# Kernel tuning notes

Hardware: AMD Instinct MI355X
Metric: run time of the kernel (lower is better)

The kernel has to match this reference:

```python
import jax, jax.numpy as jnp
import numpy as np

DIM = 256
HEADS = 4
HEAD_DIM = DIM // HEADS
SCALE = HEAD_DIM ** -0.5


def setup_inputs() -> dict:
    key = jax.random.key(0)
    k_x, k_wqkv, k_bqkv, k_wp, k_bp = jax.random.split(key, 5)
    B, N = 8, 2048
    x = jax.random.normal(k_x, (B, N, DIM), dtype=jnp.float32)
    # torch nn.Linear weights: [out_features, in_features]
    W_qkv = jax.random.normal(k_wqkv, (3 * DIM, DIM), dtype=jnp.float32) * (DIM ** -0.5)
    b_qkv = jax.random.normal(k_bqkv, (3 * DIM,), dtype=jnp.float32) * 0.02
    W_proj = jax.random.normal(k_wp, (DIM, DIM), dtype=jnp.float32) * (DIM ** -0.5)
    b_proj = jax.random.normal(k_bp, (DIM,), dtype=jnp.float32) * 0.02
    return {"x": x, "W_qkv": W_qkv, "b_qkv": b_qkv, "W_proj": W_proj, "b_proj": b_proj}


def reference(x, W_qkv, b_qkv, W_proj, b_proj):
    B, N, C = x.shape
    h, d = HEADS, HEAD_DIM
    # fused QKV projection: [B,N,3C] -> [3,B,h,N,d]
    qkv = (jnp.einsum('bnc,oc->bno', x, W_qkv) + b_qkv)
    qkv = qkv.reshape(B, N, 3, h, d).transpose(2, 0, 3, 1, 4)
    q, k, v = qkv[0], qkv[1], qkv[2]
    # full N x N score matrix, as in the original module
    attn = jnp.einsum('bhnd,bhmd->bhnm', q, k) * SCALE
    attn = jax.nn.softmax(attn, axis=-1)
    out = jnp.einsum('bhnm,bhmd->bhnd', attn, v)  # [B,h,N,d]
    out = out.transpose(0, 2, 1, 3).reshape(B, N, C)
    return jnp.einsum('bnc,oc->bno', out, W_proj) + b_proj
```

## Files before the change

kernel.cpp:

```cpp
#include <hip/hip_runtime.h>
#include <hip/hip_bf16.h>


typedef __bf16 bf16x8 __attribute__((ext_vector_type(8)));
typedef float f32x4 __attribute__((ext_vector_type(4)));
typedef float f32x16 __attribute__((ext_vector_type(16)));
typedef unsigned u32x2 __attribute__((ext_vector_type(2)));

#define MFMA16(a, b, c) __builtin_amdgcn_mfma_f32_16x16x32_bf16((a), (b), (c), 0, 0, 0)
#define MFMA32(a, b, c) __builtin_amdgcn_mfma_f32_32x32x16_bf16((a), (b), (c), 0, 0, 0)

#define C2 0.18033688011112042f

#if __has_builtin(__builtin_amdgcn_exp2f)
__device__ __forceinline__ float fexp2(float x) { return __builtin_amdgcn_exp2f(x); }
#else
__device__ __forceinline__ float fexp2(float x) {
    float r;
    asm("v_exp_f32 %0, %1" : "=v"(r) : "v"(x));
    return r;
}
#endif

__device__ __forceinline__ bf16x8 ldg8(const __bf16* p) {
    return *reinterpret_cast<const bf16x8*>(p);
}

__device__ __forceinline__ bf16x8 cvt8(const float* p) {
    const f32x4 a = *reinterpret_cast<const f32x4*>(p);
    const f32x4 b = *reinterpret_cast<const f32x4*>(p + 4);
    bf16x8 r;
    r[0] = (__bf16)a[0]; r[1] = (__bf16)a[1]; r[2] = (__bf16)a[2]; r[3] = (__bf16)a[3];
    r[4] = (__bf16)b[0]; r[5] = (__bf16)b[1]; r[6] = (__bf16)b[2]; r[7] = (__bf16)b[3];
    return r;
}

__device__ __forceinline__ unsigned pk2(float a, float b) {
    __bf16 x = (__bf16)a, y = (__bf16)b;
    unsigned short ux = __builtin_bit_cast(unsigned short, x);
    unsigned short uy = __builtin_bit_cast(unsigned short, y);
    return (unsigned)ux | ((unsigned)uy << 16);
}

__global__ __launch_bounds__(256) void cvt_all(
    const float* __restrict__ X, const float* __restrict__ Wq,
    const float* __restrict__ Wp, __bf16* __restrict__ Xb,
    __bf16* __restrict__ Wqb, __bf16* __restrict__ Wpb)
{
    const int g = blockIdx.x * 256 + threadIdx.x;
    const float* src;
    __bf16* dst;
    int off;
    if (g < 524288)      { src = X;  dst = Xb;  off = g; }
    else if (g < 548864) { src = Wq; dst = Wqb; off = g - 524288; }
    else                 { src = Wp; dst = Wpb; off = g - 548864; }
    *reinterpret_cast<bf16x8*>(dst + (size_t)off * 8) = cvt8(src + (size_t)off * 8);
}

__global__ __launch_bounds__(256) void qkv_gemm(
    const __bf16* __restrict__ X, const __bf16* __restrict__ Wq,
    const float* __restrict__ bq, __bf16* __restrict__ Qw,
    __bf16* __restrict__ Kw, __bf16* __restrict__ Vt)
{
    const int tid = threadIdx.x;
    const int w = tid >> 6, lane = tid & 63;
    const int lo = lane & 15, hi = lane >> 4;
    const int n0 = blockIdx.x * 128;
    const int m0 = blockIdx.y * 128 + w * 32;

    f32x4 acc[2][8] = {};
    const __bf16* xp = X + (m0 + lo) * 256 + hi * 8;
    const __bf16* wp = Wq + (n0 + lo) * 256 + hi * 8;
    #pragma unroll
    for (int k = 0; k < 256; k += 32) {
        bf16x8 a0 = ldg8(xp + k);
        bf16x8 a1 = ldg8(xp + 16 * 256 + k);
        #pragma unroll
        for (int f = 0; f < 8; ++f) {
            bf16x8 bf = ldg8(wp + f * 16 * 256 + k);
            acc[0][f] = MFMA16(a0, bf, acc[0][f]);
            acc[1][f] = MFMA16(a1, bf, acc[1][f]);
        }
    }

    #pragma unroll
    for (int ni = 0; ni < 8; ++ni) {
        const int col = n0 + ni * 16 + lo;
        const float bias = bq[col];
        const float scale = (col < 256) ? C2 : 1.0f;
        #pragma unroll
        for (int mi = 0; mi < 2; ++mi) {
            #pragma unroll
            for (int r = 0; r < 4; ++r) {
                const int row = m0 + mi * 16 + hi * 4 + r;
                const __bf16 hv = (__bf16)((acc[mi][ni][r] + bias) * scale);
                const int bb = row >> 11, n = row & 2047;
                const int d = col & 63;
                if (col < 256) {
                    const int h = col >> 6;
                    Qw[((bb * 4 + h) * 2048 + n) * 64 + d] = hv;
                } else if (col < 512) {
                    const int h = (col - 256) >> 6;
                    Kw[((bb * 4 + h) * 2048 + n) * 64 + d] = hv;
                } else {
                    const int h = (col - 512) >> 6;
                    Vt[((bb * 4 + h) * 64 + d) * 2048 + n] = hv;
                }
            }
        }
    }
}

__global__ __launch_bounds__(512, 4) void attn_kernel(
    const __bf16* __restrict__ Qw, const __bf16* __restrict__ Kw,
    const __bf16* __restrict__ Vt, __bf16* __restrict__ Opart,
    float* __restrict__ Lbuf)
{
    __shared__ __align__(16) char lds[33280];

    const int tid = threadIdx.x;
    const int w = tid >> 6, lane = tid & 63;
    const int l31 = lane & 31, hi5 = lane >> 5;
    const int sw = w & 3;
    const int g  = w >> 2;

    const int bid = blockIdx.x;
    const int work = (bid & 7) * 128 + (bid >> 3);
    const int bh = work >> 5;
    const int split = (work >> 4) & 1;
    const int qx = work & 15;

    const int q = qx * 128 + sw * 32 + l31;
    const int kvbase = split * 1024 + g * 512;
    const int gbase = g * 16384;

    const __bf16* Qp = Qw + (bh * 2048 + q) * 64 + hi5 * 8;
    bf16x8 Qf[4];
    #pragma unroll
    for (int db = 0; db < 4; ++db) Qf[db] = ldg8(Qp + db * 16);

    const __bf16* Kbase = Kw + (size_t)bh * 2048 * 64;
    const __bf16* Vbase = Vt + (size_t)bh * 64 * 2048;

    const int idx = tid & 255;
    const int krow = idx >> 3, kcol8 = (idx & 7) * 8;
    const int swz = ((idx >> 3) & 7) << 4;
    const int kb0 = gbase + ((idx * 16) ^ swz);
    const int kb1 = gbase + (((idx + 256) * 16) ^ swz);
    const int vb0 = gbase + 8192 + ((idx * 16) ^ swz);
    const int vb1 = gbase + 8192 + (((idx + 256) * 16) ^ swz);

    bf16x8 R0 = ldg8(Kbase + (kvbase + krow) * 64 + kcol8);
    bf16x8 R1 = ldg8(Kbase + (kvbase + krow + 32) * 64 + kcol8);
    bf16x8 R2 = ldg8(Vbase + krow * 2048 + kvbase + kcol8);
    bf16x8 R3 = ldg8(Vbase + (krow + 32) * 2048 + kvbase + kcol8);

    f32x16 oacc0 = (f32x16)0.0f, oacc1 = (f32x16)0.0f;
    float lr = 0.0f;

    for (int t = 0; t < 8; ++t) {
        *reinterpret_cast<bf16x8*>(lds + kb0) = R0;
        *reinterpret_cast<bf16x8*>(lds + kb1) = R1;
        *reinterpret_cast<bf16x8*>(lds + vb0) = R2;
        *reinterpret_cast<bf16x8*>(lds + vb1) = R3;
        __syncthreads();

        if (t < 7) {
            const int kv0n = kvbase + (t + 1) * 64;
            R0 = ldg8(Kbase + (kv0n + krow) * 64 + kcol8);
            R1 = ldg8(Kbase + (kv0n + krow + 32) * 64 + kcol8);
            R2 = ldg8(Vbase + krow * 2048 + kv0n + kcol8);
            R3 = ldg8(Vbase + (krow + 32) * 2048 + kv0n + kcol8);
        }

        f32x16 s0 = (f32x16)0.0f, s1 = (f32x16)0.0f;
        #pragma unroll
        for (int db = 0; db < 4; ++db) {
            const int colb = hi5 * 16 + db * 32;
            bf16x8 k0 = *reinterpret_cast<const bf16x8*>(
                lds + gbase + ((l31 * 128 + colb) ^ ((l31 & 7) << 4)));
            bf16x8 k1 = *reinterpret_cast<const bf16x8*>(
                lds + gbase + (((l31 + 32) * 128 + colb) ^ ((l31 & 7) << 4)));
            s0 = MFMA32(k0, Qf[db], s0);
            s1 = MFMA32(k1, Qf[db], s1);
        }

        float p0[16], p1[16];
        #pragma unroll
        for (int i = 0; i < 16; ++i) p0[i] = fexp2(s0[i]);
        #pragma unroll
        for (int i = 0; i < 16; ++i) p1[i] = fexp2(s1[i]);

        float r0 = 0.f, r1 = 0.f, r2 = 0.f, r3 = 0.f;
        #pragma unroll
        for (int i = 0; i < 4; ++i) {
            r0 += p0[i]; r1 += p0[4 + i]; r2 += p0[8 + i]; r3 += p0[12 + i];
            r0 += p1[i]; r1 += p1[4 + i]; r2 += p1[8 + i]; r3 += p1[12 + i];
        }
        lr += (r0 + r1) + (r2 + r3);

#define PVSTEP(PARR, KH)                                                      \
        {                                                                     \
            _Pragma("unroll")                                                 \
            for (int bb2 = 0; bb2 < 2; ++bb2) {                               \
                const int vcolb = KH * 64 + bb2 * 32 + hi5 * 16;              \
                bf16x8 v0 = *reinterpret_cast<const bf16x8*>(                 \
                    lds + gbase + 8192 + ((l31 * 128 + vcolb) ^ ((l31 & 7) << 4))); \
                bf16x8 v1 = *reinterpret_cast<const bf16x8*>(                 \
                    lds + gbase + 8192 + (((l31 + 32) * 128 + vcolb) ^ ((l31 & 7) << 4))); \
                unsigned w0 = pk2(PARR[8 * bb2 + 0], PARR[8 * bb2 + 1]);      \
                unsigned w1 = pk2(PARR[8 * bb2 + 2], PARR[8 * bb2 + 3]);      \
                unsigned w2 = pk2(PARR[8 * bb2 + 4], PARR[8 * bb2 + 5]);      \
                unsigned w3 = pk2(PARR[8 * bb2 + 6], PARR[8 * bb2 + 7]);      \
                asm volatile("v_permlane32_swap_b32 %0, %1" : "+v"(w0), "+v"(w2)); \
                asm volatile("v_permlane32_swap_b32 %0, %1" : "+v"(w1), "+v"(w3)); \
                union { unsigned u[4]; bf16x8 v; } pb;                        \
                pb.u[0] = w0; pb.u[1] = w1; pb.u[2] = w2; pb.u[3] = w3;       \
                oacc0 = MFMA32(v0, pb.v, oacc0);                              \
                oacc1 = MFMA32(v1, pb.v, oacc1);                              \
            }                                                                 \
        }
        PVSTEP(p0, 0)
        PVSTEP(p1, 1)
#undef PVSTEP
        __syncthreads();
    }

    lr += __shfl_xor(lr, 32);

    float* mb = reinterpret_cast<float*>(lds);
    float* lb = reinterpret_cast<float*>(lds + 32768);
    if (g == 1) {
        #pragma unroll
        for (int i = 0; i < 16; ++i) {
            const int r = (i & 3) + 8 * (i >> 2) + 4 * hi5;
            mb[(sw * 64 + r) * 32 + l31] = oacc0[i];
            mb[(sw * 64 + 32 + r) * 32 + l31] = oacc1[i];
        }
        if (hi5 == 0) lb[sw * 32 + l31] = lr;
    }
    __syncthreads();
    if (g == 0) {
        #pragma unroll
        for (int i = 0; i < 16; ++i) {
            const int r = (i & 3) + 8 * (i >> 2) + 4 * hi5;
            oacc0[i] += mb[(sw * 64 + r) * 32 + l31];
            oacc1[i] += mb[(sw * 64 + 32 + r) * 32 + l31];
        }
        lr += lb[sw * 32 + l31];

        __bf16* Od = Opart + ((size_t)(split * 32 + bh) * 2048 + q) * 64 + hi5 * 4;
#define EPI(OACC, DBLK)                                                       \
        {                                                                     \
            _Pragma("unroll")                                                 \
            for (int rq = 0; rq < 4; ++rq) {                                  \
                u32x2 st;                                                     \
                st.x = pk2(OACC[rq * 4 + 0], OACC[rq * 4 + 1]);               \
                st.y = pk2(OACC[rq * 4 + 2], OACC[rq * 4 + 3]);               \
                *reinterpret_cast<u32x2*>(Od + DBLK * 32 + rq * 8) = st;      \
            }                                                                 \
        }
        EPI(oacc0, 0)
        EPI(oacc1, 1)
#undef EPI
        if (hi5 == 0) Lbuf[(size_t)(split * 32 + bh) * 2048 + q] = lr;
    }
}

__global__ __launch_bounds__(256) void merge_kernel(
    const __bf16* __restrict__ Opart, const float* __restrict__ Lbuf,
    __bf16* __restrict__ Ow)
{
    const int g = blockIdx.x * 256 + threadIdx.x;
    const int dg = g & 7;
    const int q = (g >> 3) & 2047;
    const int bh = g >> 14;
    const float l1 = Lbuf[(size_t)bh * 2048 + q];
    const float l2 = Lbuf[(size_t)(32 + bh) * 2048 + q];
    const float inv = 1.0f / (l1 + l2);
    const __bf16* O1 = Opart + ((size_t)bh * 2048 + q) * 64 + dg * 8;
    const __bf16* O2 = O1 + (size_t)32 * 2048 * 64;
    const bf16x8 a = ldg8(O1);
    const bf16x8 b = ldg8(O2);
    bf16x8 r;
    #pragma unroll
    for (int i = 0; i < 8; ++i)
        r[i] = (__bf16)(((float)a[i] + (float)b[i]) * inv);
    const int bb = bh >> 2, h = bh & 3;
    *reinterpret_cast<bf16x8*>(Ow + ((size_t)(bb * 2048 + q)) * 256 + h * 64 + dg * 8) = r;
}

__global__ __launch_bounds__(256) void proj_gemm(
    const __bf16* __restrict__ A, const __bf16* __restrict__ Wp,
    const float* __restrict__ bp, float* __restrict__ out)
{
    const int tid = threadIdx.x;
    const int w = tid >> 6, lane = tid & 63;
    const int lo = lane & 15, hi = lane >> 4;
    const int n0 = blockIdx.x * 128;
    const int m0 = blockIdx.y * 128 + w * 32;

    f32x4 acc[2][8] = {};
    const __bf16* ap = A + (m0 + lo) * 256 + hi * 8;
    const __bf16* wp = Wp + (n0 + lo) * 256 + hi * 8;
    #pragma unroll
    for (int k = 0; k < 256; k += 32) {
        bf16x8 a0 = ldg8(ap + k);
        bf16x8 a1 = ldg8(ap + 16 * 256 + k);
        #pragma unroll
        for (int f = 0; f < 8; ++f) {
            bf16x8 bf = ldg8(wp + f * 16 * 256 + k);
            acc[0][f] = MFMA16(a0, bf, acc[0][f]);
            acc[1][f] = MFMA16(a1, bf, acc[1][f]);
        }
    }
    #pragma unroll
    for (int ni = 0; ni < 8; ++ni) {
        const int col = n0 + ni * 16 + lo;
        const float bias = bp[col];
        #pragma unroll
        for (int mi = 0; mi < 2; ++mi) {
            #pragma unroll
            for (int r = 0; r < 4; ++r) {
                const int row = m0 + mi * 16 + hi * 4 + r;
                out[row * 256 + col] = acc[mi][ni][r] + bias;
            }
        }
    }
}

extern "C" void kernel_launch(void* const* d_in, const int* in_sizes, int n_in,
                              void* d_out, int out_size, void* d_ws, size_t ws_size,
                              hipStream_t stream)
{
    const float* x  = (const float*)d_in[0];
    const float* Wq = (const float*)d_in[1];
    const float* bq = (const float*)d_in[2];
    const float* Wp = (const float*)d_in[3];
    const float* bp = (const float*)d_in[4];

    __bf16* ws = (__bf16*)d_ws;
    const size_t SZ = (size_t)32 * 2048 * 64;
    __bf16* Xb  = ws;
    __bf16* Wqb = Xb + SZ;
    __bf16* Wpb = Wqb + 196608;
    __bf16* Qw  = Wpb + 65536;
    __bf16* Kw  = Qw + SZ;
    __bf16* Vt  = Kw + SZ;
    float*  Lbuf = (float*)(Vt + SZ);
    __bf16* Ow  = Xb;

    __bf16* Opart = (__bf16*)d_out;

    cvt_all<<<2176, 256, 0, stream>>>(x, Wq, Wp, Xb, Wqb, Wpb);
    qkv_gemm<<<dim3(6, 128), 256, 0, stream>>>(Xb, Wqb, bq, Qw, Kw, Vt);
    attn_kernel<<<1024, 512, 0, stream>>>(Qw, Kw, Vt, Opart, Lbuf);
    merge_kernel<<<2048, 256, 0, stream>>>(Opart, Lbuf, Ow);
    proj_gemm<<<dim3(2, 128), 256, 0, stream>>>(Ow, Wpb, bp, (float*)d_out);
}
```

Before: 146.6 us.

## Drop KV split in attention and fuse normalization, removing merge kernel

```diff
diff --git a/kernel.cpp b/kernel.cpp
--- a/kernel.cpp
+++ b/kernel.cpp
@@ -113,8 +113,7 @@
 
 __global__ __launch_bounds__(512, 4) void attn_kernel(
     const __bf16* __restrict__ Qw, const __bf16* __restrict__ Kw,
-    const __bf16* __restrict__ Vt, __bf16* __restrict__ Opart,
-    float* __restrict__ Lbuf)
+    const __bf16* __restrict__ Vt, __bf16* __restrict__ Ow)
 {
     __shared__ __align__(16) char lds[33280];
 
@@ -125,13 +124,12 @@
     const int g  = w >> 2;
 
     const int bid = blockIdx.x;
-    const int work = (bid & 7) * 128 + (bid >> 3);
-    const int bh = work >> 5;
-    const int split = (work >> 4) & 1;
+    const int work = (bid & 7) * 64 + (bid >> 3);
+    const int bh = work >> 4;
     const int qx = work & 15;
 
     const int q = qx * 128 + sw * 32 + l31;
-    const int kvbase = split * 1024 + g * 512;
+    const int kvbase = g * 1024;
     const int gbase = g * 16384;
 
     const __bf16* Qp = Qw + (bh * 2048 + q) * 64 + hi5 * 8;
@@ -158,14 +156,14 @@
     f32x16 oacc0 = (f32x16)0.0f, oacc1 = (f32x16)0.0f;
     float lr = 0.0f;
 
-    for (int t = 0; t < 8; ++t) {
+    for (int t = 0; t < 16; ++t) {
         *reinterpret_cast<bf16x8*>(lds + kb0) = R0;
         *reinterpret_cast<bf16x8*>(lds + kb1) = R1;
         *reinterpret_cast<bf16x8*>(lds + vb0) = R2;
         *reinterpret_cast<bf16x8*>(lds + vb1) = R3;
         __syncthreads();
 
-        if (t < 7) {
+        if (t < 15) {
             const int kv0n = kvbase + (t + 1) * 64;
             R0 = ldg8(Kbase + (kv0n + krow) * 64 + kcol8);
             R1 = ldg8(Kbase + (kv0n + krow + 32) * 64 + kcol8);
@@ -249,45 +247,23 @@
         }
         lr += lb[sw * 32 + l31];
 
-        __bf16* Od = Opart + ((size_t)(split * 32 + bh) * 2048 + q) * 64 + hi5 * 4;
+        const float invl = 1.0f / lr;
+        const int bb = bh >> 2, h = bh & 3;
+        __bf16* Op = Ow + ((size_t)(bb * 2048 + q)) * 256 + h * 64 + hi5 * 4;
 #define EPI(OACC, DBLK)                                                       \
         {                                                                     \
             _Pragma("unroll")                                                 \
             for (int rq = 0; rq < 4; ++rq) {                                  \
                 u32x2 st;                                                     \
-                st.x = pk2(OACC[rq * 4 + 0], OACC[rq * 4 + 1]);               \
-                st.y = pk2(OACC[rq * 4 + 2], OACC[rq * 4 + 3]);               \
-                *reinterpret_cast<u32x2*>(Od + DBLK * 32 + rq * 8) = st;      \
+                st.x = pk2(OACC[rq * 4 + 0] * invl, OACC[rq * 4 + 1] * invl); \
+                st.y = pk2(OACC[rq * 4 + 2] * invl, OACC[rq * 4 + 3] * invl); \
+                *reinterpret_cast<u32x2*>(Op + DBLK * 32 + rq * 8) = st;      \
             }                                                                 \
         }
         EPI(oacc0, 0)
         EPI(oacc1, 1)
 #undef EPI
-        if (hi5 == 0) Lbuf[(size_t)(split * 32 + bh) * 2048 + q] = lr;
-    }
-}
-
-__global__ __launch_bounds__(256) void merge_kernel(
-    const __bf16* __restrict__ Opart, const float* __restrict__ Lbuf,
-    __bf16* __restrict__ Ow)
-{
-    const int g = blockIdx.x * 256 + threadIdx.x;
-    const int dg = g & 7;
-    const int q = (g >> 3) & 2047;
-    const int bh = g >> 14;
-    const float l1 = Lbuf[(size_t)bh * 2048 + q];
-    const float l2 = Lbuf[(size_t)(32 + bh) * 2048 + q];
-    const float inv = 1.0f / (l1 + l2);
-    const __bf16* O1 = Opart + ((size_t)bh * 2048 + q) * 64 + dg * 8;
-    const __bf16* O2 = O1 + (size_t)32 * 2048 * 64;
-    const bf16x8 a = ldg8(O1);
-    const bf16x8 b = ldg8(O2);
-    bf16x8 r;
-    #pragma unroll
-    for (int i = 0; i < 8; ++i)
-        r[i] = (__bf16)(((float)a[i] + (float)b[i]) * inv);
-    const int bb = bh >> 2, h = bh & 3;
-    *reinterpret_cast<bf16x8*>(Ow + ((size_t)(bb * 2048 + q)) * 256 + h * 64 + dg * 8) = r;
+    }
 }
 
 __global__ __launch_bounds__(256) void proj_gemm(
@@ -347,14 +323,10 @@
     __bf16* Qw  = Wpb + 65536;
     __bf16* Kw  = Qw + SZ;
     __bf16* Vt  = Kw + SZ;
-    float*  Lbuf = (float*)(Vt + SZ);
     __bf16* Ow  = Xb;
-
-    __bf16* Opart = (__bf16*)d_out;
 
     cvt_all<<<2176, 256, 0, stream>>>(x, Wq, Wp, Xb, Wqb, Wpb);
     qkv_gemm<<<dim3(6, 128), 256, 0, stream>>>(Xb, Wqb, bq, Qw, Kw, Vt);
-    attn_kernel<<<1024, 512, 0, stream>>>(Qw, Kw, Vt, Opart, Lbuf);
-    merge_kernel<<<2048, 256, 0, stream>>>(Opart, Lbuf, Ow);
+    attn_kernel<<<512, 512, 0, stream>>>(Qw, Kw, Vt, Ow);
     proj_gemm<<<dim3(2, 128), 256, 0, stream>>>(Ow, Wpb, bp, (float*)d_out);
 }
```

New measurement: 128.4 us. -12.4%, faster.
